# Optimization experiments

Measured on AMD Instinct MI355X. Metric: run time of the kernel, lower is better.

Reference implementation:

```python
import jax, jax.numpy as jnp
import numpy as np

WS = 8   # window_size
NH = 4   # num_heads
EPS = 1e-5

def _rel_pos_index(ws):
    # Static Swin relative-position index, computed with numpy (constant).
    coords = np.stack(np.meshgrid(np.arange(ws), np.arange(ws), indexing='ij'))  # [2,ws,ws]
    cf = coords.reshape(2, -1)                       # [2, N]
    rel = cf[:, :, None] - cf[:, None, :]            # [2, N, N]
    rel = rel.transpose(1, 2, 0).copy()              # [N, N, 2]
    rel[:, :, 0] += ws - 1
    rel[:, :, 1] += ws - 1
    rel[:, :, 0] *= 2 * ws - 1
    return jnp.asarray(rel.sum(-1))                  # [N, N] int

def setup_inputs() -> dict:
    key = jax.random.key(0)
    ks = jax.random.split(key, 4)
    B, C, H, W = 8, 64, 256, 256
    return {
        'x': jax.random.normal(ks[0], (B, C, H, W), jnp.float32),
        'norm_w': jnp.ones((C,), jnp.float32),
        'norm_b': jnp.zeros((C,), jnp.float32),
        'qkv_w': jax.random.normal(ks[1], (3 * C, C), jnp.float32) * 0.05,
        'proj_w': jax.random.normal(ks[2], (C, C), jnp.float32) * 0.05,
        'attn_scale': jnp.ones((1,), jnp.float32) * 0.2,
        'rpb_table': jax.random.normal(ks[3], ((2 * WS - 1) ** 2, NH), jnp.float32) * 0.02,
    }

def reference(x, norm_w, norm_b, qkv_w, proj_w, attn_scale, rpb_table):
    B, C, H, W = x.shape
    ws, nh = WS, NH
    hd = C // nh
    N = ws * ws
    nwh, nww = H // ws, W // ws  # H,W multiples of ws -> pad branch is a no-op
    # window partition: [B,C,H,W] -> [B*nwh*nww, N, C]
    xw = x.reshape(B, C, nwh, ws, nww, ws).transpose(0, 2, 4, 3, 5, 1).reshape(-1, N, C)
    # LayerNorm over channels
    mu = xw.mean(-1, keepdims=True)
    var = xw.var(-1, keepdims=True)
    xn = (xw - mu) / jnp.sqrt(var + EPS) * norm_w + norm_b
    # qkv projection (torch Linear: y = x @ W.T), split heads
    qkv = (xn @ qkv_w.T).reshape(-1, N, 3, nh, hd).transpose(2, 0, 3, 1, 4)  # [3, Wn, h, N, hd]
    q, k, v = qkv[0], qkv[1], qkv[2]
    attn = jnp.einsum('whnd,whmd->whnm', q, k) * (hd ** -0.5)  # [Wn, h, N, N]
    # gathered relative position bias
    rpi = _rel_pos_index(ws)                      # [N, N]
    bias = rpb_table[rpi].transpose(2, 0, 1)      # [h, N, N]
    attn = jax.nn.softmax(attn + bias[None], axis=-1)
    out = jnp.einsum('whnm,whmd->whnd', attn, v)  # [Wn, h, N, hd]
    out = out.transpose(0, 2, 1, 3).reshape(-1, N, C)
    out = out @ proj_w.T
    # window reverse: -> [B, C, H, W]
    out = out.reshape(B, nwh, nww, ws, ws, C).transpose(0, 5, 1, 3, 2, 4).reshape(B, C, H, W)
    return x + attn_scale * out
```

## Files before the change

kernel.cpp:

```cpp
#include <hip/hip_runtime.h>
#include <hip/hip_bf16.h>

#define WSZ 8
#define NHE 4
#define CH 64

typedef unsigned short u16;
typedef unsigned int u32;
typedef __attribute__((ext_vector_type(8))) short short8;
typedef __attribute__((ext_vector_type(4))) short short4v;
typedef __attribute__((ext_vector_type(4))) float float4v;

__device__ __forceinline__ u16 f2bf(float f) {
    __hip_bfloat16 h = __float2bfloat16(f);
    return __builtin_bit_cast(u16, h);
}
__device__ __forceinline__ int SW(int row, int col) {
    return row * 64 + (col ^ ((row & 7) << 3));
}

#define MFMA(a, b, c) __builtin_amdgcn_mfma_f32_16x16x32_bf16(a, b, c, 0, 0, 0)
#define QKSC 0.36067376022224085f

__global__ void prep(const float* __restrict__ qkvw, const float* __restrict__ projw,
                     const float* __restrict__ rpb,
                     u16* __restrict__ wq, u16* __restrict__ wp, float* __restrict__ bl)
{
    int t = blockIdx.x * 256 + threadIdx.x;
    if (t < 12288) {
        int j = t & 7, nl = (t >> 3) & 15, q = (t >> 7) & 3, kt = (t >> 9) & 1, nt = t >> 10;
        wq[t] = f2bf(qkvw[(nt * 16 + nl) * CH + kt * 32 + q * 8 + j]);
    }
    if (t < 4096) {
        int j = t & 7, nl = (t >> 3) & 15, q = (t >> 7) & 3, kt = (t >> 9) & 1, wv = t >> 10;
        wp[t] = f2bf(projw[(wv * 16 + nl) * CH + kt * 32 + q * 8 + j]);
    }
    if (t < 16384) {
        int r = t & 3, nt = (t >> 2) & 3, lane = (t >> 4) & 63, mt = (t >> 10) & 3, h = t >> 12;
        int nl = lane & 15, q = lane >> 4;
        int tokm = mt * 16 + nl, tokn = nt * 16 + q * 4 + r;
        int im = tokm >> 3, jm = tokm & 7, in_ = tokn >> 3, jn = tokn & 7;
        bl[t] = rpb[((im - in_ + 7) * 15 + (jm - jn + 7)) * NHE + h] * 1.44269504088896341f;
    }
}

__global__ __launch_bounds__(256, 6) void win_attn(
    const float* __restrict__ x, const float* __restrict__ nw, const float* __restrict__ nb,
    const u16* __restrict__ wq, const u16* __restrict__ wp,
    const float* __restrict__ ascale, const float* __restrict__ biasl,
    float* __restrict__ out, int B, int H, int W)
{
    const int HWsz = H * W;
    const int nww = W / WSZ, nwh = H / WSZ;
    const int win = (blockIdx.x & 7) * ((int)gridDim.x >> 3) + (blockIdx.x >> 3);
    const int ww = win % nww;
    const int t1 = win / nww;
    const int wh = t1 % nwh;
    const int b  = t1 / nwh;

    const int tid  = threadIdx.x;
    const int lane = tid & 63;
    const int wv   = tid >> 6;
    const int q    = lane >> 4;
    const int nl   = lane & 15;

    __shared__ alignas(16) char smem[24576];
    u16*   XN  = (u16*)(smem);
    u16*   QO  = (u16*)(smem);
    u16*   KS  = (u16*)(smem + 8192);
    u16*   VS  = (u16*)(smem + 16384);
    float* PS  = (float*)(smem + 16384);
    float* PS2 = PS + 256;

    const int rowbase = (wh * WSZ) * W + ww * WSZ;
    const float* xw = x + (size_t)b * CH * HWsz + rowbase;
    const int tokoff = (lane >> 3) * W + (lane & 7);

    float xv[16];
    {
        const float* xc = xw + (size_t)(wv * 16) * HWsz + tokoff;
        #pragma unroll
        for (int ci = 0; ci < 16; ci++) xv[ci] = xc[(size_t)ci * HWsz];
        float s = 0.f, s2 = 0.f;
        #pragma unroll
        for (int ci = 0; ci < 16; ci++) { s += xv[ci]; s2 += xv[ci] * xv[ci]; }
        PS[wv * 64 + lane] = s;
        PS2[wv * 64 + lane] = s2;
    }
    __syncthreads();

    {
        float s  = PS[lane]  + PS[64 + lane]  + PS[128 + lane]  + PS[192 + lane];
        float s2 = PS2[lane] + PS2[64 + lane] + PS2[128 + lane] + PS2[192 + lane];
        float mu  = s * (1.f / 64.f);
        float var = s2 * (1.f / 64.f) - mu * mu;
        float rs  = rsqrtf(var + 1e-5f);
        float v[16];
        #pragma unroll
        for (int ci = 0; ci < 16; ci++) {
            int c = wv * 16 + ci;
            v[ci] = (xv[ci] - mu) * rs * nw[c] + nb[c];
        }
        #pragma unroll
        for (int g = 0; g < 2; g++) {
            short8 pk;
            #pragma unroll
            for (int j = 0; j < 8; j++) pk[j] = (short)f2bf(v[g * 8 + j]);
            *(short8*)&XN[lane * 64 + ((wv * 16 + g * 8) ^ ((lane & 7) << 3))] = pk;
        }
    }
    __syncthreads();

    short8 afr[4][2];
    #pragma unroll
    for (int mt = 0; mt < 4; mt++)
        #pragma unroll
        for (int kt = 0; kt < 2; kt++) {
            int m = mt * 16 + nl;
            int phys = (kt * 4 + q) ^ (m & 7);
            afr[mt][kt] = *(short8*)&XN[m * 64 + phys * 8];
        }
    short8 bfrs[3][2];
    #pragma unroll
    for (int nt3 = 0; nt3 < 3; nt3++) {
        int nt = wv * 3 + nt3;
        #pragma unroll
        for (int kt = 0; kt < 2; kt++)
            bfrs[nt3][kt] = *(const short8*)&wq[((((nt * 2 + kt) * 4 + q) * 16) + nl) * 8];
    }
    __syncthreads();

    #pragma unroll
    for (int nt3 = 0; nt3 < 3; nt3++) {
        int nt = wv * 3 + nt3;
        int which = nt >> 2;
        int chb = (nt & 3) * 16 + nl;
        #pragma unroll
        for (int mt = 0; mt < 4; mt++) {
            float4v acc = {0.f, 0.f, 0.f, 0.f};
            acc = MFMA(afr[mt][0], bfrs[nt3][0], acc);
            acc = MFMA(afr[mt][1], bfrs[nt3][1], acc);
            int tok0 = mt * 16 + q * 4;
            if (which == 0) {
                #pragma unroll
                for (int r = 0; r < 4; r++) QO[SW(tok0 + r, chb)] = f2bf(acc[r]);
            } else if (which == 1) {
                #pragma unroll
                for (int r = 0; r < 4; r++) KS[SW(tok0 + r, chb)] = f2bf(acc[r]);
            } else {
                short4v pk;
                pk[0] = (short)f2bf(acc[0]); pk[1] = (short)f2bf(acc[1]);
                pk[2] = (short)f2bf(acc[2]); pk[3] = (short)f2bf(acc[3]);
                int pt = tok0 ^ ((chb & 7) << 3);
                *(short4v*)&VS[chb * 64 + pt] = pk;
            }
        }
    }
    __syncthreads();

    {
        const int h = wv;
        const short8 zero8 = {0, 0, 0, 0, 0, 0, 0, 0};
        short8 kfr[4], vfr[2];
        #pragma unroll
        for (int nt = 0; nt < 4; nt++) {
            if (q < 2) {
                int n = nt * 16 + nl;
                int phys = (h * 2 + q) ^ (n & 7);
                kfr[nt] = *(short8*)&KS[n * 64 + phys * 8];
            } else kfr[nt] = zero8;
        }
        #pragma unroll
        for (int kt = 0; kt < 2; kt++) {
            int c = h * 16 + nl;
            int phys = (kt * 4 + q) ^ (c & 7);
            vfr[kt] = *(short8*)&VS[c * 64 + phys * 8];
        }
        u16* Pw = VS + h * 1024;
        #pragma unroll
        for (int mt = 0; mt < 4; mt++) {
            short8 qf;
            if (q < 2) {
                int m = mt * 16 + nl;
                int phys = (h * 2 + q) ^ (m & 7);
                qf = *(short8*)&QO[m * 64 + phys * 8];
            } else qf = zero8;
            const float4v* bp = (const float4v*)(biasl + ((((h * 4 + mt) * 64) + lane) << 4));
            float4v sacc[4];
            #pragma unroll
            for (int nt = 0; nt < 4; nt++) {
                float4v z = {0.f, 0.f, 0.f, 0.f};
                sacc[nt] = MFMA(kfr[nt], qf, z);
            }
            float p[16], mx = -1e30f;
            #pragma unroll
            for (int nt = 0; nt < 4; nt++) {
                float4v blv = bp[nt];
                #pragma unroll
                for (int r = 0; r < 4; r++) {
                    float s = fmaf(sacc[nt][r], QKSC, blv[r]);
                    p[nt * 4 + r] = s;
                    mx = fmaxf(mx, s);
                }
            }
            mx = fmaxf(mx, __shfl_xor(mx, 16, 64));
            mx = fmaxf(mx, __shfl_xor(mx, 32, 64));
            float sum = 0.f;
            #pragma unroll
            for (int i = 0; i < 16; i++) {
                float e = __builtin_amdgcn_exp2f(p[i] - mx);
                p[i] = e;
                sum += e;
            }
            sum += __shfl_xor(sum, 16, 64);
            sum += __shfl_xor(sum, 32, 64);
            float inv = __builtin_amdgcn_rcpf(sum);
            #pragma unroll
            for (int nt = 0; nt < 4; nt++)
                #pragma unroll
                for (int r = 0; r < 4; r++)
                    Pw[SW(nl, nt * 16 + q * 4 + r)] = f2bf(p[nt * 4 + r] * inv);
            float4v oacc = {0.f, 0.f, 0.f, 0.f};
            #pragma unroll
            for (int kt = 0; kt < 2; kt++) {
                int phys = (kt * 4 + q) ^ (nl & 7);
                short8 pf = *(short8*)&Pw[nl * 64 + phys * 8];
                oacc = MFMA(pf, vfr[kt], oacc);
            }
            #pragma unroll
            for (int r = 0; r < 4; r++)
                QO[SW(mt * 16 + q * 4 + r, h * 16 + nl)] = f2bf(oacc[r]);
        }
    }
    __syncthreads();

    {
        const float asc = ascale[0];
        const int ch = wv * 16 + nl;
        const float* xrp = xw + (size_t)ch * HWsz;
        float4v xr[4];
        #pragma unroll
        for (int mt = 0; mt < 4; mt++) {
            int tok0 = mt * 16 + q * 4;
            xr[mt] = *(const float4v*)(xrp + (tok0 >> 3) * W + (tok0 & 7));
        }
        short8 wfr[2];
        #pragma unroll
        for (int kt = 0; kt < 2; kt++)
            wfr[kt] = *(const short8*)&wp[((((wv * 2 + kt) * 4 + q) * 16) + nl) * 8];
        float* outp = out + ((size_t)b * CH + ch) * HWsz + rowbase;
        #pragma unroll
        for (int mt = 0; mt < 4; mt++) {
            float4v yacc = {0.f, 0.f, 0.f, 0.f};
            #pragma unroll
            for (int kt = 0; kt < 2; kt++) {
                int m = mt * 16 + nl;
                int phys = (kt * 4 + q) ^ (m & 7);
                short8 of = *(short8*)&QO[m * 64 + phys * 8];
                yacc = MFMA(of, wfr[kt], yacc);
            }
            int tok0 = mt * 16 + q * 4;
            int i = tok0 >> 3, j = tok0 & 7;
            float4v y;
            y[0] = xr[mt][0] + asc * yacc[0];
            y[1] = xr[mt][1] + asc * yacc[1];
            y[2] = xr[mt][2] + asc * yacc[2];
            y[3] = xr[mt][3] + asc * yacc[3];
            *(float4v*)(outp + i * W + j) = y;
        }
    }
}

extern "C" void kernel_launch(void* const* d_in, const int* in_sizes, int n_in,
                              void* d_out, int out_size, void* d_ws, size_t ws_size,
                              hipStream_t stream) {
    const float* x     = (const float*)d_in[0];
    const float* nw    = (const float*)d_in[1];
    const float* nb    = (const float*)d_in[2];
    const float* qkvw  = (const float*)d_in[3];
    const float* projw = (const float*)d_in[4];
    const float* asc   = (const float*)d_in[5];
    const float* rpb   = (const float*)d_in[6];

    const int H = 256, W = 256;
    const int B = in_sizes[0] / (CH * H * W);
    const int nwin = B * (H / WSZ) * (W / WSZ);

    u16*   wq = (u16*)d_ws;
    u16*   wp = (u16*)((char*)d_ws + 24576);
    float* bl = (float*)((char*)d_ws + 32768);

    prep<<<64, 256, 0, stream>>>(qkvw, projw, rpb, wq, wp, bl);
    win_attn<<<nwin, 256, 0, stream>>>(x, nw, nb, wq, wp, asc, bl,
                                       (float*)d_out, B, H, W);
}
```

Before: 364.5 us.

## Process two adjacent windows per 512-thread block and prefetch residual early

```diff
diff --git a/kernel.cpp b/kernel.cpp
--- a/kernel.cpp
+++ b/kernel.cpp
@@ -44,48 +44,53 @@
     }
 }
 
-__global__ __launch_bounds__(256, 6) void win_attn(
+__global__ __launch_bounds__(512, 6) void win_attn(
     const float* __restrict__ x, const float* __restrict__ nw, const float* __restrict__ nb,
     const u16* __restrict__ wq, const u16* __restrict__ wp,
     const float* __restrict__ ascale, const float* __restrict__ biasl,
     float* __restrict__ out, int B, int H, int W)
 {
     const int HWsz = H * W;
-    const int nww = W / WSZ, nwh = H / WSZ;
-    const int win = (blockIdx.x & 7) * ((int)gridDim.x >> 3) + (blockIdx.x >> 3);
-    const int ww = win % nww;
-    const int t1 = win / nww;
-    const int wh = t1 % nwh;
-    const int b  = t1 / nwh;
+    const int nww = W / WSZ, nwh = H / WSZ, npr = nww >> 1;
+    const int NBLK = (int)gridDim.x;
+    const int pw = (blockIdx.x & 7) * (NBLK >> 3) + ((int)blockIdx.x >> 3);
+    const int wwp = pw % npr;
+    const int t1  = pw / npr;
+    const int wh  = t1 % nwh;
+    const int b   = t1 / nwh;
 
     const int tid  = threadIdx.x;
     const int lane = tid & 63;
     const int wv   = tid >> 6;
+    const int ws   = wv >> 2;
+    const int wvl  = wv & 3;
     const int q    = lane >> 4;
     const int nl   = lane & 15;
 
-    __shared__ alignas(16) char smem[24576];
-    u16*   XN  = (u16*)(smem);
-    u16*   QO  = (u16*)(smem);
-    u16*   KS  = (u16*)(smem + 8192);
-    u16*   VS  = (u16*)(smem + 16384);
-    float* PS  = (float*)(smem + 16384);
+    __shared__ alignas(16) char smem[49152];
+    char* sm = smem + ws * 24576;
+    u16*   XN  = (u16*)(sm);
+    u16*   QO  = (u16*)(sm);
+    u16*   KS  = (u16*)(sm + 8192);
+    u16*   VS  = (u16*)(sm + 16384);
+    float* PS  = (float*)(sm + 16384);
     float* PS2 = PS + 256;
 
+    const int ww = wwp * 2 + ws;
     const int rowbase = (wh * WSZ) * W + ww * WSZ;
     const float* xw = x + (size_t)b * CH * HWsz + rowbase;
     const int tokoff = (lane >> 3) * W + (lane & 7);
 
     float xv[16];
     {
-        const float* xc = xw + (size_t)(wv * 16) * HWsz + tokoff;
+        const float* xc = xw + (size_t)(wvl * 16) * HWsz + tokoff;
         #pragma unroll
         for (int ci = 0; ci < 16; ci++) xv[ci] = xc[(size_t)ci * HWsz];
         float s = 0.f, s2 = 0.f;
         #pragma unroll
         for (int ci = 0; ci < 16; ci++) { s += xv[ci]; s2 += xv[ci] * xv[ci]; }
-        PS[wv * 64 + lane] = s;
-        PS2[wv * 64 + lane] = s2;
+        PS[wvl * 64 + lane] = s;
+        PS2[wvl * 64 + lane] = s2;
     }
     __syncthreads();
 
@@ -98,7 +103,7 @@
         float v[16];
         #pragma unroll
         for (int ci = 0; ci < 16; ci++) {
-            int c = wv * 16 + ci;
+            int c = wvl * 16 + ci;
             v[ci] = (xv[ci] - mu) * rs * nw[c] + nb[c];
         }
         #pragma unroll
@@ -106,7 +111,7 @@
             short8 pk;
             #pragma unroll
             for (int j = 0; j < 8; j++) pk[j] = (short)f2bf(v[g * 8 + j]);
-            *(short8*)&XN[lane * 64 + ((wv * 16 + g * 8) ^ ((lane & 7) << 3))] = pk;
+            *(short8*)&XN[lane * 64 + ((wvl * 16 + g * 8) ^ ((lane & 7) << 3))] = pk;
         }
     }
     __syncthreads();
@@ -123,16 +128,26 @@
     short8 bfrs[3][2];
     #pragma unroll
     for (int nt3 = 0; nt3 < 3; nt3++) {
-        int nt = wv * 3 + nt3;
+        int nt = wvl * 3 + nt3;
         #pragma unroll
         for (int kt = 0; kt < 2; kt++)
             bfrs[nt3][kt] = *(const short8*)&wq[((((nt * 2 + kt) * 4 + q) * 16) + nl) * 8];
     }
+    const int ch = wvl * 16 + nl;
+    float4v xr[4];
+    {
+        const float* xrp = xw + (size_t)ch * HWsz;
+        #pragma unroll
+        for (int mt = 0; mt < 4; mt++) {
+            int tok0 = mt * 16 + q * 4;
+            xr[mt] = *(const float4v*)(xrp + (tok0 >> 3) * W + (tok0 & 7));
+        }
+    }
     __syncthreads();
 
     #pragma unroll
     for (int nt3 = 0; nt3 < 3; nt3++) {
-        int nt = wv * 3 + nt3;
+        int nt = wvl * 3 + nt3;
         int which = nt >> 2;
         int chb = (nt & 3) * 16 + nl;
         #pragma unroll
@@ -159,7 +174,7 @@
     __syncthreads();
 
     {
-        const int h = wv;
+        const int h = wvl;
         const short8 zero8 = {0, 0, 0, 0, 0, 0, 0, 0};
         short8 kfr[4], vfr[2];
         #pragma unroll
@@ -236,18 +251,10 @@
 
     {
         const float asc = ascale[0];
-        const int ch = wv * 16 + nl;
-        const float* xrp = xw + (size_t)ch * HWsz;
-        float4v xr[4];
-        #pragma unroll
-        for (int mt = 0; mt < 4; mt++) {
-            int tok0 = mt * 16 + q * 4;
-            xr[mt] = *(const float4v*)(xrp + (tok0 >> 3) * W + (tok0 & 7));
-        }
         short8 wfr[2];
         #pragma unroll
         for (int kt = 0; kt < 2; kt++)
-            wfr[kt] = *(const short8*)&wp[((((wv * 2 + kt) * 4 + q) * 16) + nl) * 8];
+            wfr[kt] = *(const short8*)&wp[((((wvl * 2 + kt) * 4 + q) * 16) + nl) * 8];
         float* outp = out + ((size_t)b * CH + ch) * HWsz + rowbase;
         #pragma unroll
         for (int mt = 0; mt < 4; mt++) {
@@ -285,12 +292,13 @@
     const int H = 256, W = 256;
     const int B = in_sizes[0] / (CH * H * W);
     const int nwin = B * (H / WSZ) * (W / WSZ);
+    const int nblk = nwin / 2;
 
     u16*   wq = (u16*)d_ws;
     u16*   wp = (u16*)((char*)d_ws + 24576);
     float* bl = (float*)((char*)d_ws + 32768);
 
     prep<<<64, 256, 0, stream>>>(qkvw, projw, rpb, wq, wp, bl);
-    win_attn<<<nwin, 256, 0, stream>>>(x, nw, nb, wq, wp, asc, bl,
+    win_attn<<<nblk, 512, 0, stream>>>(x, nw, nb, wq, wp, asc, bl,
                                        (float*)d_out, B, H, W);
 }
```

Result: slower. 475.2 us (+30.4%).

## Give each wave a private per-head Q/K/V tile and drop a block barrier

Applied to the files above, without the earlier changes.

```diff
diff --git a/kernel.cpp b/kernel.cpp
--- a/kernel.cpp
+++ b/kernel.cpp
@@ -6,7 +6,6 @@
 #define CH 64
 
 typedef unsigned short u16;
-typedef unsigned int u32;
 typedef __attribute__((ext_vector_type(8))) short short8;
 typedef __attribute__((ext_vector_type(4))) short short4v;
 typedef __attribute__((ext_vector_type(4))) float float4v;
@@ -44,7 +43,7 @@
     }
 }
 
-__global__ __launch_bounds__(256, 6) void win_attn(
+__global__ __launch_bounds__(256, 5) void win_attn(
     const float* __restrict__ x, const float* __restrict__ nw, const float* __restrict__ nb,
     const u16* __restrict__ wq, const u16* __restrict__ wp,
     const float* __restrict__ ascale, const float* __restrict__ biasl,
@@ -64,12 +63,12 @@
     const int q    = lane >> 4;
     const int nl   = lane & 15;
 
-    __shared__ alignas(16) char smem[24576];
+    __shared__ alignas(16) char smem[32768];
     u16*   XN  = (u16*)(smem);
-    u16*   QO  = (u16*)(smem);
-    u16*   KS  = (u16*)(smem + 8192);
-    u16*   VS  = (u16*)(smem + 16384);
-    float* PS  = (float*)(smem + 16384);
+    u16*   QW  = (u16*)(smem + 8192) + wv * 3072;
+    u16*   KW  = QW + 1024;
+    u16*   VW  = QW + 2048;
+    float* PS  = (float*)(smem + 8192);
     float* PS2 = PS + 256;
 
     const int rowbase = (wh * WSZ) * W + ww * WSZ;
@@ -123,7 +122,7 @@
     short8 bfrs[3][2];
     #pragma unroll
     for (int nt3 = 0; nt3 < 3; nt3++) {
-        int nt = wv * 3 + nt3;
+        int nt = wv + nt3 * 4;
         #pragma unroll
         for (int kt = 0; kt < 2; kt++)
             bfrs[nt3][kt] = *(const short8*)&wq[((((nt * 2 + kt) * 4 + q) * 16) + nl) * 8];
@@ -132,59 +131,44 @@
 
     #pragma unroll
     for (int nt3 = 0; nt3 < 3; nt3++) {
-        int nt = wv * 3 + nt3;
-        int which = nt >> 2;
-        int chb = (nt & 3) * 16 + nl;
         #pragma unroll
         for (int mt = 0; mt < 4; mt++) {
             float4v acc = {0.f, 0.f, 0.f, 0.f};
             acc = MFMA(afr[mt][0], bfrs[nt3][0], acc);
             acc = MFMA(afr[mt][1], bfrs[nt3][1], acc);
             int tok0 = mt * 16 + q * 4;
-            if (which == 0) {
-                #pragma unroll
-                for (int r = 0; r < 4; r++) QO[SW(tok0 + r, chb)] = f2bf(acc[r]);
-            } else if (which == 1) {
-                #pragma unroll
-                for (int r = 0; r < 4; r++) KS[SW(tok0 + r, chb)] = f2bf(acc[r]);
+            if (nt3 == 0) {
+                #pragma unroll
+                for (int r = 0; r < 4; r++) QW[(tok0 + r) * 16 + nl] = f2bf(acc[r]);
+            } else if (nt3 == 1) {
+                #pragma unroll
+                for (int r = 0; r < 4; r++) KW[(tok0 + r) * 16 + nl] = f2bf(acc[r]);
             } else {
                 short4v pk;
                 pk[0] = (short)f2bf(acc[0]); pk[1] = (short)f2bf(acc[1]);
                 pk[2] = (short)f2bf(acc[2]); pk[3] = (short)f2bf(acc[3]);
-                int pt = tok0 ^ ((chb & 7) << 3);
-                *(short4v*)&VS[chb * 64 + pt] = pk;
-            }
-        }
-    }
-    __syncthreads();
+                int pt = tok0 ^ ((nl & 7) << 3);
+                *(short4v*)&VW[nl * 64 + pt] = pk;
+            }
+        }
+    }
 
     {
         const int h = wv;
         const short8 zero8 = {0, 0, 0, 0, 0, 0, 0, 0};
         short8 kfr[4], vfr[2];
         #pragma unroll
-        for (int nt = 0; nt < 4; nt++) {
-            if (q < 2) {
-                int n = nt * 16 + nl;
-                int phys = (h * 2 + q) ^ (n & 7);
-                kfr[nt] = *(short8*)&KS[n * 64 + phys * 8];
-            } else kfr[nt] = zero8;
-        }
+        for (int nt = 0; nt < 4; nt++)
+            kfr[nt] = (q < 2) ? *(short8*)&KW[(nt * 16 + nl) * 16 + q * 8] : zero8;
         #pragma unroll
         for (int kt = 0; kt < 2; kt++) {
-            int c = h * 16 + nl;
-            int phys = (kt * 4 + q) ^ (c & 7);
-            vfr[kt] = *(short8*)&VS[c * 64 + phys * 8];
-        }
-        u16* Pw = VS + h * 1024;
-        #pragma unroll
-        for (int mt = 0; mt < 4; mt++) {
-            short8 qf;
-            if (q < 2) {
-                int m = mt * 16 + nl;
-                int phys = (h * 2 + q) ^ (m & 7);
-                qf = *(short8*)&QO[m * 64 + phys * 8];
-            } else qf = zero8;
+            int phys = (kt * 4 + q) ^ (nl & 7);
+            vfr[kt] = *(short8*)&VW[nl * 64 + phys * 8];
+        }
+        u16* Pw = KW;
+        #pragma unroll
+        for (int mt = 0; mt < 4; mt++) {
+            short8 qf = (q < 2) ? *(short8*)&QW[(mt * 16 + nl) * 16 + q * 8] : zero8;
             const float4v* bp = (const float4v*)(biasl + ((((h * 4 + mt) * 64) + lane) << 4));
             float4v sacc[4];
             #pragma unroll
@@ -229,7 +213,7 @@
             }
             #pragma unroll
             for (int r = 0; r < 4; r++)
-                QO[SW(mt * 16 + q * 4 + r, h * 16 + nl)] = f2bf(oacc[r]);
+                XN[SW(mt * 16 + q * 4 + r, h * 16 + nl)] = f2bf(oacc[r]);
         }
     }
     __syncthreads();
@@ -256,7 +240,7 @@
             for (int kt = 0; kt < 2; kt++) {
                 int m = mt * 16 + nl;
                 int phys = (kt * 4 + q) ^ (m & 7);
-                short8 of = *(short8*)&QO[m * 64 + phys * 8];
+                short8 of = *(short8*)&XN[m * 64 + phys * 8];
                 yacc = MFMA(of, wfr[kt], yacc);
             }
             int tok0 = mt * 16 + q * 4;
```

Measured after the change: 330.2 us. 1.1x faster.
